# Performance work log

Measured on AMD Instinct MI355X. Metric: run time of the kernel, lower is better.

Reference implementation:

```python
import jax, jax.numpy as jnp
import numpy as np

DIM = 2048
N_HEADS = 16
HEAD_DIM = DIM // N_HEADS  # 128
B, S = 2, 2048


def setup_inputs() -> dict:
    key = jax.random.key(0)
    ks = jax.random.split(key, 12)
    sc = 1.0 / np.sqrt(DIM)
    inp = {
        "x": jax.random.normal(ks[0], (B, S, DIM), jnp.float32),
        # freqs for rotary: angle theta per (position, pair)
        "freqs_cos": jnp.cos(jnp.outer(jnp.arange(S, dtype=jnp.float32),
                                        1.0 / (10000.0 ** (jnp.arange(0, HEAD_DIM, 2, dtype=jnp.float32) / HEAD_DIM)))),
        "freqs_sin": jnp.sin(jnp.outer(jnp.arange(S, dtype=jnp.float32),
                                        1.0 / (10000.0 ** (jnp.arange(0, HEAD_DIM, 2, dtype=jnp.float32) / HEAD_DIM)))),
        "wq_w": jax.random.normal(ks[1], (DIM, DIM), jnp.float32) * sc,
        "wq_b": jax.random.normal(ks[2], (DIM,), jnp.float32) * sc,
        "wk_w": jax.random.normal(ks[3], (DIM, DIM), jnp.float32) * sc,
        "wk_b": jax.random.normal(ks[4], (DIM,), jnp.float32) * sc,
        "wv_w": jax.random.normal(ks[5], (DIM, DIM), jnp.float32) * sc,
        "wv_b": jax.random.normal(ks[6], (DIM,), jnp.float32) * sc,
        "wo_w": jax.random.normal(ks[7], (DIM, DIM), jnp.float32) * sc,
        "wo_b": jax.random.normal(ks[8], (DIM,), jnp.float32) * sc,
    }
    return inp


def _rope(xq, xk, cos, sin):
    # xq/xk: [B, S, H, D]; cos/sin: [S, D//2]
    def rot(t):
        tr = t.reshape(*t.shape[:-1], -1, 2)  # [B,S,H,D//2,2]
        t0, t1 = tr[..., 0], tr[..., 1]
        c = cos[None, :, None, :]
        s = sin[None, :, None, :]
        o0 = t0 * c - t1 * s
        o1 = t0 * s + t1 * c
        return jnp.stack([o0, o1], axis=-1).reshape(t.shape)
    return rot(xq), rot(xk)


def reference(x, freqs_cos, freqs_sin, wq_w, wq_b, wk_w, wk_b, wv_w, wv_b, wo_w, wo_b):
    b, s, _ = x.shape
    xq = (x @ wq_w.T + wq_b).reshape(b, s, N_HEADS, HEAD_DIM)
    xk = (x @ wk_w.T + wk_b).reshape(b, s, N_HEADS, HEAD_DIM)
    xv = (x @ wv_w.T + wv_b).reshape(b, s, N_HEADS, HEAD_DIM)
    xq, xk = _rope(xq, xk, freqs_cos, freqs_sin)
    # NOTE: original has NO softmax — raw scaled scores are used directly.
    scores = jnp.einsum('bqhd,bkhd->bhqk', xq, xk) / jnp.sqrt(jnp.float32(HEAD_DIM))
    out = jnp.einsum('bhqk,bkhd->bqhd', scores, xv).reshape(b, s, DIM)
    return out @ wo_w.T + wo_b
```

## Files before the change

kernel.cpp:

```cpp
#include <hip/hip_runtime.h>
#include <hip/hip_bf16.h>

#define DIMN 2048
#define NQKV 6144
#define NH 16
#define HD 128
#define BSZ 2
#define SEQ 2048
#define ROWS (BSZ*SEQ)

typedef short short8 __attribute__((ext_vector_type(8)));
typedef float f32x4 __attribute__((ext_vector_type(4)));

__device__ __forceinline__ unsigned short f2bf(float f) {
    __hip_bfloat16 h = __float2bfloat16(f);
    unsigned short u; __builtin_memcpy(&u, &h, 2); return u;
}

__device__ __forceinline__ void gld_lds16(const void* g, void* l) {
    __builtin_amdgcn_global_load_lds(
        (const __attribute__((address_space(1))) void*)g,
        (__attribute__((address_space(3))) void*)l, 16, 0, 0);
}

__global__ void cvt_all(const float* __restrict__ x, const float* __restrict__ wq,
                        const float* __restrict__ wk, const float* __restrict__ wv,
                        const float* __restrict__ wo,
                        unsigned short* __restrict__ Xb, unsigned short* __restrict__ Wcat,
                        unsigned short* __restrict__ Wo2) {
    int bid = blockIdx.x;
    const float* in; unsigned short* out; int base;
    if      (bid <  8192) { in = x;  out = Xb;             base = bid; }
    else if (bid < 12288) { in = wq; out = Wcat;           base = bid - 8192; }
    else if (bid < 16384) { in = wk; out = Wcat + 4194304; base = bid - 12288; }
    else if (bid < 20480) { in = wv; out = Wcat + 8388608; base = bid - 16384; }
    else                  { in = wo; out = Wo2;            base = bid - 20480; }
    int i = (base * 256 + threadIdx.x) * 4;
    float4 v = *(const float4*)(in + i);
    ushort4 o; o.x = f2bf(v.x); o.y = f2bf(v.y); o.z = f2bf(v.z); o.w = f2bf(v.w);
    *(ushort4*)(out + i) = o;
}


template<int MODE>
__global__ __launch_bounds__(512, 2) void gemm256(
    const unsigned short* __restrict__ A, int lda,
    const unsigned short* __restrict__ B, int ldb,
    const float* __restrict__ b0, const float* __restrict__ b1, const float* __restrict__ b2,
    const float* __restrict__ fcos, const float* __restrict__ fsin,
    void* __restrict__ C, int ldc, int K)
{
    __shared__ __align__(16) unsigned short As[32768];
    __shared__ __align__(16) unsigned short Bs[32768];

    const int t  = threadIdx.x;
    const int l  = t & 63;
    const int w  = t >> 6;
    const int wr = w >> 2;
    const int wc = w & 3;
    const int fr = l & 15, fq = l >> 4;

    const int xcd = blockIdx.x & 7;
    const int j   = blockIdx.x >> 3;
    int mt, nt;
    if (MODE == 0) {
        if (j < 32) { mt = (xcd & 1) * 8 + (j >> 2); nt = (xcd >> 1) * 4 + (j & 3); }
        else { const int p = j - 32, c = xcd >> 1;
               mt = (c & 1) * 8 + (xcd & 1) * 4 + (p >> 2); nt = (4 + (c >> 1)) * 4 + (p & 3); }
    } else {
        mt = (xcd >> 1) * 4 + (j >> 2);
        nt = (xcd & 1) * 4 + (j & 3);
    }
    const int m0 = mt * 256;
    const int n0 = nt * 256;

    const unsigned short* Bsel = B;
    if (MODE == 1 && m0 >= 2048) Bsel += (size_t)2048 * 2048;

    const int srow = t >> 3;
    const int scol = ((t & 7) ^ (srow & 7)) * 8;
    const unsigned short* aS = A    + (size_t)(m0 + srow) * lda + scol;
    const unsigned short* bS = Bsel + (size_t)(n0 + srow) * ldb + scol;

#define STG_A(KT, H) do { \
    const unsigned short* s_ = aS + (size_t)(H) * 128 * lda + (size_t)(KT) * 64; \
    gld_lds16(s_,                    &As[(((KT) & 1) << 14) + ((H) << 13) + t * 8]); \
    gld_lds16(s_ + (size_t)64 * lda, &As[(((KT) & 1) << 14) + ((H) << 13) + 4096 + t * 8]); \
  } while (0)
#define STG_B(KT, H) do { \
    const unsigned short* s_ = bS + (size_t)(H) * 128 * ldb + (size_t)(KT) * 64; \
    gld_lds16(s_,                    &Bs[(((KT) & 1) << 14) + ((H) << 13) + t * 8]); \
    gld_lds16(s_ + (size_t)64 * ldb, &Bs[(((KT) & 1) << 14) + ((H) << 13) + 4096 + t * 8]); \
  } while (0)

    const int cK0 = (fq ^ (fr & 7)) * 8;
    const int cK1 = ((4 + fq) ^ (fr & 7)) * 8;
    const int aB0 = wr * 8192 + fr * 64;
    const int bB0 = wc * 4096 + fr * 64;

    const unsigned aA0 = (unsigned)(size_t)&As[aB0 + cK0];
    const unsigned aA1 = (unsigned)(size_t)&As[aB0 + cK1];
    const unsigned bA0 = (unsigned)(size_t)&Bs[bB0 + cK0];
    const unsigned bA1 = (unsigned)(size_t)&Bs[bB0 + cK1];

    short8 aF[4][2], bF0[2][2], bF1[2][2];
    f32x4  acc[8][4] = {};

#define DSR(dst, areg, OFF) \
    asm volatile("ds_read_b128 %0, %1 offset:%2" : "=v"(dst) : "v"(areg), "n"(OFF))

#define RD_A(DDB, QM) do { \
    DSR(aF[0][0], aA0, (DDB) + (QM) * 8192 + 0);    DSR(aF[0][1], aA1, (DDB) + (QM) * 8192 + 0); \
    DSR(aF[1][0], aA0, (DDB) + (QM) * 8192 + 2048); DSR(aF[1][1], aA1, (DDB) + (QM) * 8192 + 2048); \
    DSR(aF[2][0], aA0, (DDB) + (QM) * 8192 + 4096); DSR(aF[2][1], aA1, (DDB) + (QM) * 8192 + 4096); \
    DSR(aF[3][0], aA0, (DDB) + (QM) * 8192 + 6144); DSR(aF[3][1], aA1, (DDB) + (QM) * 8192 + 6144); \
  } while (0)
#define RD_B(DDB, QN, BF) do { \
    DSR(BF[0][0], bA0, (DDB) + (QN) * 4096 + 0);    DSR(BF[0][1], bA1, (DDB) + (QN) * 4096 + 0); \
    DSR(BF[1][0], bA0, (DDB) + (QN) * 4096 + 2048); DSR(BF[1][1], bA1, (DDB) + (QN) * 4096 + 2048); \
  } while (0)

#define BAR() asm volatile("s_barrier" ::: "memory")

#define MM(QM, QN, BF) do { \
    _Pragma("unroll") for (int m2 = 0; m2 < 4; ++m2) \
      _Pragma("unroll") for (int n2 = 0; n2 < 2; ++n2) { \
        acc[(QM)*4+m2][(QN)*2+n2] = __builtin_amdgcn_mfma_f32_16x16x32_bf16( \
            aF[m2][0], BF[n2][0], acc[(QM)*4+m2][(QN)*2+n2], 0, 0, 0); \
        acc[(QM)*4+m2][(QN)*2+n2] = __builtin_amdgcn_mfma_f32_16x16x32_bf16( \
            aF[m2][1], BF[n2][1], acc[(QM)*4+m2][(QN)*2+n2], 0, 0, 0); } \
  } while (0)

#define TILE(KT, DDB) do { \
    if ((KT) + 1 < ktT) { \
        STG_A((KT) + 1, 0); STG_A((KT) + 1, 1); \
        STG_B((KT) + 1, 0); STG_B((KT) + 1, 1); \
    } \
    RD_A(DDB, 0); RD_B(DDB, 0, bF0); RD_B(DDB, 1, bF1); \
    asm volatile("s_waitcnt lgkmcnt(4)"); \
    __builtin_amdgcn_sched_barrier(0); \
    __builtin_amdgcn_s_setprio(1); \
    MM(0, 0, bF0); \
    asm volatile("s_waitcnt lgkmcnt(0)"); \
    __builtin_amdgcn_sched_barrier(0); \
    MM(0, 1, bF1); \
    __builtin_amdgcn_s_setprio(0); \
    RD_A(DDB, 1); \
    asm volatile("s_waitcnt lgkmcnt(0)"); \
    __builtin_amdgcn_sched_barrier(0); \
    __builtin_amdgcn_s_setprio(1); \
    MM(1, 0, bF0); MM(1, 1, bF1); \
    __builtin_amdgcn_s_setprio(0); \
    asm volatile("s_waitcnt vmcnt(0)"); \
    __builtin_amdgcn_sched_barrier(0); \
    BAR(); \
  } while (0)

    const int ktT = K >> 6;

    STG_A(0, 0); STG_A(0, 1);
    STG_B(0, 0); STG_B(0, 1);
    asm volatile("s_waitcnt vmcnt(0)");
    __builtin_amdgcn_sched_barrier(0);
    BAR();

    for (int kt = 0; kt < ktT; kt += 2) {
        TILE(kt, 0);
        TILE(kt + 1, 32768);
    }

#undef TILE
#undef MM
#undef BAR
#undef RD_A
#undef RD_B
#undef DSR
#undef STG_A
#undef STG_B

    #pragma unroll
    for (int mi = 0; mi < 8; ++mi) {
        #pragma unroll
        for (int ni = 0; ni < 4; ++ni) {
            #pragma unroll
            for (int j2 = 0; j2 < 4; ++j2) {
                const int r  = m0 + wr * 128 + mi * 16 + fq * 4 + j2;
                const int cg = n0 + wc * 64 + ni * 16 + fr;
                float v = acc[mi][ni][j2];
                if (MODE == 0) {
                    v += (cg < 2048) ? b0[cg] : ((cg < 4096) ? b1[cg - 2048] : b2[cg - 4096]);
                    if (cg < 4096) {
                        const int s = r & (SEQ - 1);
                        const int i = (cg >> 1) & 63;
                        const float cs = fcos[s * 64 + i];
                        const float sn = fsin[s * 64 + i];
                        const float p  = __shfl_xor(v, 1);
                        v = (fr & 1) ? (p * sn + v * cs) : (v * cs - p * sn);
                    }
                    ((unsigned short*)C)[(size_t)r * ldc + cg] = f2bf(v);
                } else {
                    v += b0[cg];
                    ((float*)C)[(size_t)r * ldc + cg] = v;
                }
            }
        }
    }
}

template<int OUT_BF16, int HAS_BIAS>
__device__ __forceinline__ void gemm_tile_core(
    const unsigned short* __restrict__ A, int lda,
    const unsigned short* __restrict__ B, int ldb,
    const float* __restrict__ bias,
    void* __restrict__ Cptr, int ldc, int K)
{
    __shared__ __align__(16) unsigned short As[128 * 64];
    __shared__ __align__(16) unsigned short Bs[128 * 64];

    const int t  = threadIdx.x;
    const int l  = t & 63;
    const int w  = t >> 6;
    const int wr = w >> 1, wc = w & 1;
    const int fr = l & 15, fq = l >> 4;

    f32x4 acc[4][4] = {};

    const int srow = t >> 3;
    const int scol = (t & 7) * 8;

    for (int k0 = 0; k0 < K; k0 += 64) {
        __syncthreads();
        #pragma unroll
        for (int r = 0; r < 4; ++r) {
            gld_lds16(A + (size_t)(r * 32 + srow) * lda + k0 + scol, &As[(r * 32 + srow) * 64 + scol]);
            gld_lds16(B + (size_t)(r * 32 + srow) * ldb + k0 + scol, &Bs[(r * 32 + srow) * 64 + scol]);
        }
        __syncthreads();
        #pragma unroll
        for (int kk = 0; kk < 2; ++kk) {
            short8 a[4], b[4];
            #pragma unroll
            for (int mi = 0; mi < 4; ++mi)
                a[mi] = *(const short8*)&As[(wr * 64 + mi * 16 + fr) * 64 + kk * 32 + fq * 8];
            #pragma unroll
            for (int ni = 0; ni < 4; ++ni)
                b[ni] = *(const short8*)&Bs[(wc * 64 + ni * 16 + fr) * 64 + kk * 32 + fq * 8];
            #pragma unroll
            for (int mi = 0; mi < 4; ++mi)
                #pragma unroll
                for (int ni = 0; ni < 4; ++ni)
                    acc[mi][ni] = __builtin_amdgcn_mfma_f32_16x16x32_bf16(a[mi], b[ni], acc[mi][ni], 0, 0, 0);
        }
    }

    #pragma unroll
    for (int mi = 0; mi < 4; ++mi) {
        #pragma unroll
        for (int ni = 0; ni < 4; ++ni) {
            #pragma unroll
            for (int j = 0; j < 4; ++j) {
                int rr = wr * 64 + mi * 16 + fq * 4 + j;
                int cc = wc * 64 + ni * 16 + fr;
                float v = acc[mi][ni][j];
                if (HAS_BIAS) v += bias[cc];
                if (OUT_BF16) ((unsigned short*)Cptr)[(size_t)rr * ldc + cc] = f2bf(v);
                else          ((float*)Cptr)[(size_t)rr * ldc + cc] = v;
            }
        }
    }
}

__global__ __launch_bounds__(256) void ktv_kernel(
    const unsigned short* __restrict__ QKV, float* __restrict__ part)
{
    const int ks = blockIdx.x;
    const int bh = blockIdx.y;
    const int b = bh >> 4, h = bh & 15;
    const unsigned short* Kbase = QKV + (size_t)(b * SEQ + ks * 256) * NQKV + 2048 + h * HD;
    const unsigned short* Vbase = QKV + (size_t)(b * SEQ + ks * 256) * NQKV + 4096 + h * HD;

    __shared__ __align__(16) unsigned short Ks_[64 * 128];
    __shared__ __align__(16) unsigned short Vs_[64 * 128];

    const int t  = threadIdx.x;
    const int l  = t & 63;
    const int w  = t >> 6;
    const int wr = w >> 1, wc = w & 1;
    const int fr = l & 15, fq = l >> 4;

    f32x4 acc[4][4] = {};

    const int srow = t >> 4;
    const int scol = (t & 15) * 8;

    for (int sc = 0; sc < 4; ++sc) {
        __syncthreads();
        #pragma unroll
        for (int r = 0; r < 4; ++r) {
            gld_lds16(Kbase + (size_t)(sc * 64 + r * 16 + srow) * NQKV + scol, &Ks_[(r * 16 + srow) * 128 + scol]);
            gld_lds16(Vbase + (size_t)(sc * 64 + r * 16 + srow) * NQKV + scol, &Vs_[(r * 16 + srow) * 128 + scol]);
        }
        __syncthreads();
        #pragma unroll
        for (int kk = 0; kk < 2; ++kk) {
            short8 a[4], bb[4];
            #pragma unroll
            for (int mi = 0; mi < 4; ++mi)
                #pragma unroll
                for (int i = 0; i < 8; ++i)
                    a[mi][i] = (short)Ks_[(kk * 32 + fq * 8 + i) * 128 + wr * 64 + mi * 16 + fr];
            #pragma unroll
            for (int ni = 0; ni < 4; ++ni)
                #pragma unroll
                for (int i = 0; i < 8; ++i)
                    bb[ni][i] = (short)Vs_[(kk * 32 + fq * 8 + i) * 128 + wc * 64 + ni * 16 + fr];
            #pragma unroll
            for (int mi = 0; mi < 4; ++mi)
                #pragma unroll
                for (int ni = 0; ni < 4; ++ni)
                    acc[mi][ni] = __builtin_amdgcn_mfma_f32_16x16x32_bf16(a[mi], bb[ni], acc[mi][ni], 0, 0, 0);
        }
    }

    float* base = part + ((size_t)bh * 8 + ks) * 16384;
    #pragma unroll
    for (int mi = 0; mi < 4; ++mi)
        #pragma unroll
        for (int ni = 0; ni < 4; ++ni)
            #pragma unroll
            for (int j = 0; j < 4; ++j)
                base[(wr * 64 + mi * 16 + fq * 4 + j) * 128 + wc * 64 + ni * 16 + fr] = acc[mi][ni][j];
}

__global__ void ktv_reduce(const float* __restrict__ part, unsigned short* __restrict__ M2t) {
    int idx = blockIdx.x * 256 + threadIdx.x;
    int bh = idx >> 14, rem = idx & 16383;
    const float* p = part + ((size_t)bh * 8) * 16384 + rem;
    float s = 0.f;
    #pragma unroll
    for (int k = 0; k < 8; ++k) s += p[(size_t)k * 16384];
    M2t[idx] = f2bf(s * 0.08838834764831845f);
}

__global__ __launch_bounds__(256) void w2_gemm(
    const unsigned short* __restrict__ Wo2, const unsigned short* __restrict__ M2t,
    unsigned short* __restrict__ W2)
{
    const int mt = blockIdx.x;
    const int bh = blockIdx.y;
    const int b = bh >> 4, h = bh & 15;
    const unsigned short* A = Wo2 + (size_t)(mt * 128) * DIMN + h * HD;
    const unsigned short* B = M2t + (size_t)bh * HD * HD;
    unsigned short* Cp = W2 + (size_t)b * DIMN * DIMN + (size_t)(mt * 128) * DIMN + h * HD;
    gemm_tile_core<1, 0>(A, DIMN, B, HD, nullptr, Cp, DIMN, HD);
}

extern "C" void kernel_launch(void* const* d_in, const int* in_sizes, int n_in,
                              void* d_out, int out_size, void* d_ws, size_t ws_size,
                              hipStream_t stream) {
    const float* x    = (const float*)d_in[0];
    const float* fcos = (const float*)d_in[1];
    const float* fsin = (const float*)d_in[2];
    const float* wq   = (const float*)d_in[3];
    const float* bq   = (const float*)d_in[4];
    const float* wk   = (const float*)d_in[5];
    const float* bk   = (const float*)d_in[6];
    const float* wv   = (const float*)d_in[7];
    const float* bv   = (const float*)d_in[8];
    const float* wo   = (const float*)d_in[9];
    const float* bo   = (const float*)d_in[10];
    float* out = (float*)d_out;

    char* ws = (char*)d_ws;
    size_t off = 0;
    auto alloc = [&](size_t bytes) { char* p = ws + off; off += (bytes + 255) & ~(size_t)255; return p; };

    unsigned short* Xb   = (unsigned short*)alloc((size_t)ROWS * DIMN * 2);
    unsigned short* Wcat = (unsigned short*)alloc((size_t)NQKV * DIMN * 2);
    unsigned short* Wo2  = (unsigned short*)alloc((size_t)DIMN * DIMN * 2);
    unsigned short* QKV  = (unsigned short*)alloc((size_t)ROWS * NQKV * 2);
    float*          part = (float*)alloc((size_t)32 * 8 * HD * HD * 4);
    unsigned short* M2t  = (unsigned short*)alloc((size_t)32 * HD * HD * 2);
    unsigned short* W2   = (unsigned short*)alloc((size_t)BSZ * DIMN * DIMN * 2);

    cvt_all<<<24576, 256, 0, stream>>>(x, wq, wk, wv, wo, Xb, Wcat, Wo2);

    gemm256<0><<<384, 512, 0, stream>>>(
        Xb, DIMN, Wcat, DIMN, bq, bk, bv, fcos, fsin, QKV, NQKV, DIMN);

    ktv_kernel<<<dim3(8, 32), 256, 0, stream>>>(QKV, part);
    ktv_reduce<<<(32 * 16384) / 256, 256, 0, stream>>>(part, M2t);

    w2_gemm<<<dim3(16, 32), 256, 0, stream>>>(Wo2, M2t, W2);

    gemm256<1><<<128, 512, 0, stream>>>(
        QKV, NQKV, W2, DIMN, bo, nullptr, nullptr, nullptr, nullptr, out, DIMN, DIMN);
}
```

Measured before the change: 228.8 us.

## Replace QKV projection GEMM with 128x128-tile 32x32x16 MFMA kernel

The fused QKV projection (4096x6144x2048) moves from the 256x256-tile, 512-thread double-buffered kernel to a new 128x128-tile, 256-thread kernel. The new kernel uses 32x32x16 bf16 MFMA and a single-buffered LDS loop with two barriers per k-step. It launches 1536 blocks instead of 384, aiming for better load balance across CUs and XCDs. The trade is lost overlap between global loads and compute, and lower per-block data reuse. The output-projection GEMM is de-templated into a specialised fp32-output kernel.

After: 261.9 us (median of 2 runs). 1.14x slower.

```diff
diff --git a/kernel.cpp b/kernel.cpp
--- a/kernel.cpp
+++ b/kernel.cpp
@@ -11,6 +11,7 @@
 
 typedef short short8 __attribute__((ext_vector_type(8)));
 typedef float f32x4 __attribute__((ext_vector_type(4)));
+typedef float f32x16 __attribute__((ext_vector_type(16)));
 
 __device__ __forceinline__ unsigned short f2bf(float f) {
     __hip_bfloat16 h = __float2bfloat16(f);
@@ -41,14 +42,92 @@
     *(ushort4*)(out + i) = o;
 }
 
-
-template<int MODE>
-__global__ __launch_bounds__(512, 2) void gemm256(
+__global__ __launch_bounds__(256) void gemm97q(
     const unsigned short* __restrict__ A, int lda,
     const unsigned short* __restrict__ B, int ldb,
     const float* __restrict__ b0, const float* __restrict__ b1, const float* __restrict__ b2,
     const float* __restrict__ fcos, const float* __restrict__ fsin,
-    void* __restrict__ C, int ldc, int K)
+    unsigned short* __restrict__ C, int ldc, int K)
+{
+    __shared__ __align__(16) unsigned short As[128 * 64];
+    __shared__ __align__(16) unsigned short Bs[128 * 64];
+
+    const int t    = threadIdx.x;
+    const int l    = t & 63;
+    const int w    = t >> 6;
+    const int wr   = w >> 1, wc = w & 1;
+    const int lrow = l & 31;
+    const int lk   = l >> 5;
+
+    const int xcd = blockIdx.x & 7;
+    const int j   = blockIdx.x >> 3;
+    const int nt  = xcd * 6 + j % 6;
+    const int mt  = j / 6;
+    const int m0 = mt * 128;
+    const int n0 = nt * 128;
+
+    const int srow = t >> 3;
+    const int scol = ((t & 7) ^ (srow & 7)) * 8;
+    const unsigned short* aS = A + (size_t)(m0 + srow) * lda + scol;
+    const unsigned short* bS = B + (size_t)(n0 + srow) * ldb + scol;
+
+    f32x16 acc[2][2] = {};
+
+    for (int k0 = 0; k0 < K; k0 += 64) {
+        __syncthreads();
+        #pragma unroll
+        for (int r = 0; r < 4; ++r) {
+            gld_lds16(aS + (size_t)(r * 32) * lda + k0, &As[r * 2048 + t * 8]);
+            gld_lds16(bS + (size_t)(r * 32) * ldb + k0, &Bs[r * 2048 + t * 8]);
+        }
+        __syncthreads();
+        #pragma unroll
+        for (int ks = 0; ks < 4; ++ks) {
+            const int co = (((ks << 1) | lk) ^ (l & 7)) * 8;
+            short8 a[2], b[2];
+            #pragma unroll
+            for (int mi = 0; mi < 2; ++mi)
+                a[mi] = *(const short8*)&As[(wr * 64 + mi * 32 + lrow) * 64 + co];
+            #pragma unroll
+            for (int ni = 0; ni < 2; ++ni)
+                b[ni] = *(const short8*)&Bs[(wc * 64 + ni * 32 + lrow) * 64 + co];
+            #pragma unroll
+            for (int mi = 0; mi < 2; ++mi)
+                #pragma unroll
+                for (int ni = 0; ni < 2; ++ni)
+                    acc[mi][ni] = __builtin_amdgcn_mfma_f32_32x32x16_bf16(a[mi], b[ni], acc[mi][ni], 0, 0, 0);
+        }
+    }
+
+    #pragma unroll
+    for (int mi = 0; mi < 2; ++mi) {
+        #pragma unroll
+        for (int ni = 0; ni < 2; ++ni) {
+            const int cg = n0 + wc * 64 + ni * 32 + lrow;
+            #pragma unroll
+            for (int reg = 0; reg < 16; ++reg) {
+                const int r = m0 + wr * 64 + mi * 32 + (reg & 3) + 8 * (reg >> 2) + 4 * lk;
+                float v = acc[mi][ni][reg];
+                v += (cg < 2048) ? b0[cg] : ((cg < 4096) ? b1[cg - 2048] : b2[cg - 4096]);
+                if (cg < 4096) {
+                    const int s = r & (SEQ - 1);
+                    const int i = (cg >> 1) & 63;
+                    const float cs = fcos[s * 64 + i];
+                    const float sn = fsin[s * 64 + i];
+                    const float p  = __shfl_xor(v, 1);
+                    v = (l & 1) ? (p * sn + v * cs) : (v * cs - p * sn);
+                }
+                C[(size_t)r * ldc + cg] = f2bf(v);
+            }
+        }
+    }
+}
+
+__global__ __launch_bounds__(512, 2) void gemm256o(
+    const unsigned short* __restrict__ A, int lda,
+    const unsigned short* __restrict__ B, int ldb,
+    const float* __restrict__ b0,
+    float* __restrict__ C, int ldc, int K)
 {
     __shared__ __align__(16) unsigned short As[32768];
     __shared__ __align__(16) unsigned short Bs[32768];
@@ -62,20 +141,13 @@
 
     const int xcd = blockIdx.x & 7;
     const int j   = blockIdx.x >> 3;
-    int mt, nt;
-    if (MODE == 0) {
-        if (j < 32) { mt = (xcd & 1) * 8 + (j >> 2); nt = (xcd >> 1) * 4 + (j & 3); }
-        else { const int p = j - 32, c = xcd >> 1;
-               mt = (c & 1) * 8 + (xcd & 1) * 4 + (p >> 2); nt = (4 + (c >> 1)) * 4 + (p & 3); }
-    } else {
-        mt = (xcd >> 1) * 4 + (j >> 2);
-        nt = (xcd & 1) * 4 + (j & 3);
-    }
+    const int mt  = (xcd >> 1) * 4 + (j >> 2);
+    const int nt  = (xcd & 1) * 4 + (j & 3);
     const int m0 = mt * 256;
     const int n0 = nt * 256;
 
     const unsigned short* Bsel = B;
-    if (MODE == 1 && m0 >= 2048) Bsel += (size_t)2048 * 2048;
+    if (m0 >= 2048) Bsel += (size_t)2048 * 2048;
 
     const int srow = t >> 3;
     const int scol = ((t & 7) ^ (srow & 7)) * 8;
@@ -186,22 +258,7 @@
             for (int j2 = 0; j2 < 4; ++j2) {
                 const int r  = m0 + wr * 128 + mi * 16 + fq * 4 + j2;
                 const int cg = n0 + wc * 64 + ni * 16 + fr;
-                float v = acc[mi][ni][j2];
-                if (MODE == 0) {
-                    v += (cg < 2048) ? b0[cg] : ((cg < 4096) ? b1[cg - 2048] : b2[cg - 4096]);
-                    if (cg < 4096) {
-                        const int s = r & (SEQ - 1);
-                        const int i = (cg >> 1) & 63;
-                        const float cs = fcos[s * 64 + i];
-                        const float sn = fsin[s * 64 + i];
-                        const float p  = __shfl_xor(v, 1);
-                        v = (fr & 1) ? (p * sn + v * cs) : (v * cs - p * sn);
-                    }
-                    ((unsigned short*)C)[(size_t)r * ldc + cg] = f2bf(v);
-                } else {
-                    v += b0[cg];
-                    ((float*)C)[(size_t)r * ldc + cg] = v;
-                }
+                C[(size_t)r * ldc + cg] = acc[mi][ni][j2] + b0[cg];
             }
         }
     }
@@ -385,7 +442,7 @@
 
     cvt_all<<<24576, 256, 0, stream>>>(x, wq, wk, wv, wo, Xb, Wcat, Wo2);
 
-    gemm256<0><<<384, 512, 0, stream>>>(
+    gemm97q<<<1536, 256, 0, stream>>>(
         Xb, DIMN, Wcat, DIMN, bq, bk, bv, fcos, fsin, QKV, NQKV, DIMN);
 
     ktv_kernel<<<dim3(8, 32), 256, 0, stream>>>(QKV, part);
@@ -393,6 +450,6 @@
 
     w2_gemm<<<dim3(16, 32), 256, 0, stream>>>(Wo2, M2t, W2);
 
-    gemm256<1><<<128, 512, 0, stream>>>(
-        QKV, NQKV, W2, DIMN, bo, nullptr, nullptr, nullptr, nullptr, out, DIMN, DIMN);
-}
+    gemm256o<<<128, 512, 0, stream>>>(
+        QKV, NQKV, W2, DIMN, bo, out, DIMN, DIMN);
+}
```
